# Performance work log

Hardware: AMD Instinct MI355X
Metric: run time of the kernel (lower is better)

## Reference

```python
import jax, jax.numpy as jnp
import numpy as np


def _dequantize_and_unpack(packed, scales):
    """packed: [d_out, d_in//2] int8, each byte holds two 4-bit nibbles.
    Returns [d_out, d_in] in scales.dtype, scaled per output row."""
    low = (packed & 15).astype(jnp.int8)
    high = (packed >> 4).astype(jnp.int8)  # arithmetic shift, like torch int8 >> 4
    low = jnp.where(low > 7, low - 16, low)
    high = jnp.where(high > 7, high - 16, high)
    # interleave: even cols = high nibble, odd cols = low nibble
    w = jnp.stack([high, low], axis=-1).reshape(packed.shape[0], -1)
    return w.astype(scales.dtype) * scales


def setup_inputs() -> dict:
    key = jax.random.key(0)
    ks = jax.random.split(key, 7)
    d = 4096
    N = 4096
    x = jax.random.normal(ks[0], (N, d), dtype=jnp.float32)
    fc1_weights_packed = jax.random.randint(ks[1], (2 * d, d // 2), -8, 7, dtype=jnp.int32).astype(jnp.int8)
    fc1_scales = (jax.random.normal(ks[2], (2 * d, 1), dtype=jnp.float32) * 0.02).astype(jnp.float16)
    fc1_bias = jax.random.normal(ks[3], (2 * d,), dtype=jnp.float32)
    fc2_weights_packed = jax.random.randint(ks[4], (d, d), -8, 7, dtype=jnp.int32).astype(jnp.int8)
    fc2_scales = (jax.random.normal(ks[5], (d, 1), dtype=jnp.float32) * 0.02).astype(jnp.float16)
    fc2_bias = jax.random.normal(ks[6], (d,), dtype=jnp.float32)
    return {
        "x": x,
        "fc1_weights_packed": fc1_weights_packed,
        "fc1_scales": fc1_scales,
        "fc1_bias": fc1_bias,
        "fc2_weights_packed": fc2_weights_packed,
        "fc2_scales": fc2_scales,
        "fc2_bias": fc2_bias,
    }


def reference(x, fc1_weights_packed, fc1_scales, fc1_bias,
              fc2_weights_packed, fc2_scales, fc2_bias):
    # fc1: dequantize to [2d, d], linear, relu
    w1 = _dequantize_and_unpack(fc1_weights_packed, fc1_scales).astype(x.dtype)
    h = jax.nn.relu(jnp.dot(x, w1.T) + fc1_bias)
    # fc2: dequantize to [d, 2d], linear
    w2 = _dequantize_and_unpack(fc2_weights_packed, fc2_scales).astype(x.dtype)
    return jnp.dot(h, w2.T) + fc2_bias
```

## Files before the change

### kernel.cpp

```cpp
#include <hip/hip_runtime.h>
#include <hip/hip_fp16.h>
#include <stdint.h>


typedef __attribute__((ext_vector_type(4)))  int i32x4;
typedef __attribute__((ext_vector_type(16))) int i32x16;
typedef __attribute__((ext_vector_type(8))) _Float16 f16x8;

__device__ __forceinline__ void load_lds16(const void* g, void* l) {
    __builtin_amdgcn_global_load_lds(
        (__attribute__((address_space(1))) void*)(void*)g,
        (__attribute__((address_space(3))) void*)(void*)l,
        16, 0, 0);
}

__device__ __forceinline__ float block_max(float m, int tid) {
    __shared__ float red[4];
#pragma unroll
    for (int off = 32; off; off >>= 1)
        m = fmaxf(m, __shfl_down(m, off, 64));
    if ((tid & 63) == 0) red[tid >> 6] = m;
    __syncthreads();
    m = fmaxf(fmaxf(red[0], red[1]), fmaxf(red[2], red[3]));
    __syncthreads();
    return m;
}

__global__ __launch_bounds__(256) void quant_x(
    const float* __restrict__ in, int* __restrict__ out,
    float* __restrict__ rscale, int ncols)
{
    const int tid = threadIdx.x;
    const int row = blockIdx.x;
    const float4* rp = (const float4*)(in + (size_t)row * ncols);
    const int nf4 = ncols / 4;
    float4 v[4];
    float m = 0.f;
#pragma unroll
    for (int k = 0; k < 4; ++k) {
        v[k] = rp[k * 256 + tid];
        m = fmaxf(m, fmaxf(fmaxf(fabsf(v[k].x), fabsf(v[k].y)),
                           fmaxf(fabsf(v[k].z), fabsf(v[k].w))));
    }
    m = block_max(m, tid);
    m = fmaxf(m, 1e-20f);
    const float inv = 127.f / m;
    if (tid == 0) rscale[row] = m / 127.f;
    int* orow = out + (size_t)row * nf4;
#pragma unroll
    for (int k = 0; k < 4; ++k) {
        int q0 = __float2int_rn(v[k].x * inv);
        int q1 = __float2int_rn(v[k].y * inv);
        int q2 = __float2int_rn(v[k].z * inv);
        int q3 = __float2int_rn(v[k].w * inv);
        orow[k * 256 + tid] = (q0 & 0xFF) | ((q1 & 0xFF) << 8) |
                              ((q2 & 0xFF) << 16) | ((q3 & 0xFF) << 24);
    }
}

__global__ __launch_bounds__(256) void quant_h(
    const _Float16* __restrict__ in, int2* __restrict__ out,
    float* __restrict__ rscale, int ncols)
{
    const int tid = threadIdx.x;
    const int row = blockIdx.x;
    const f16x8* rp = (const f16x8*)(in + (size_t)row * ncols);
    const int nv = ncols / 8;
    f16x8 v[4];
    float m = 0.f;
#pragma unroll
    for (int k = 0; k < 4; ++k) {
        v[k] = rp[k * 256 + tid];
#pragma unroll
        for (int e = 0; e < 8; ++e) m = fmaxf(m, (float)v[k][e]);
    }
    m = block_max(m, tid);
    m = fmaxf(m, 1e-20f);
    const float inv = 255.f / m;
    if (tid == 0) rscale[row] = m / 255.f;
    int2* orow = out + (size_t)row * nv;
#pragma unroll
    for (int k = 0; k < 4; ++k) {
        union { int8_t b[8]; int2 w; } u;
#pragma unroll
        for (int e = 0; e < 8; ++e) {
            int q = __float2int_rn((float)v[k][e] * inv);
            q = q < 0 ? 0 : (q > 255 ? 255 : q);
            u.b[e] = (int8_t)(q - 128);
        }
        orow[k * 256 + tid] = u.w;
    }
}

__global__ __launch_bounds__(256) void expand_int4_i8(
    const int4* __restrict__ packed, int2* __restrict__ out,
    int* __restrict__ wsum, int n_i4)
{
    const int tid = threadIdx.x;
    const int row = blockIdx.x;
    const int4* prow = packed + (size_t)row * n_i4;
    int2* orow = out + (size_t)row * n_i4;
    int sum = 0;
    for (int j = tid; j < n_i4; j += 256) {
        int4 p = prow[j];
        int vals[4] = {p.x, p.y, p.z, p.w};
        union { int8_t b[8]; int2 w; } u;
#pragma unroll
        for (int b = 0; b < 4; ++b) {
            int by = (int)(int8_t)(vals[b] & 0xFF);
            int hi = by >> 4;
            int lo = ((by & 15) ^ 8) - 8;
            u.b[2 * b] = (int8_t)hi;
            u.b[2 * b + 1] = (int8_t)lo;
            sum += hi + lo;
        }
        orow[j] = u.w;
    }
    __shared__ int sred[4];
#pragma unroll
    for (int off = 32; off; off >>= 1) sum += __shfl_down(sum, off, 64);
    if ((tid & 63) == 0) sred[tid >> 6] = sum;
    __syncthreads();
    if (tid == 0) wsum[row] = sred[0] + sred[1] + sred[2] + sred[3];
}

template <bool RELU, bool SHIFT, typename OutT>
__global__ __launch_bounds__(256) void gemm_i8(
    const int8_t* __restrict__ A, const int8_t* __restrict__ B,
    OutT* __restrict__ C,
    const float* __restrict__ sa,
    const float* __restrict__ s,
    const float* __restrict__ bias,
    const int* __restrict__ wsum,
    int M, int N, int K)
{
    __shared__ alignas(16) char sA[128 * 128];
    __shared__ alignas(16) char sB[128 * 128];

    const int tid  = threadIdx.x;
    const int lane = tid & 63;
    const int wave = tid >> 6;
    const int wm = wave & 1;
    const int wn = wave >> 1;

    const int bm = blockIdx.y * 128;
    const int bn = blockIdx.x * 128;

    const int srow = lane >> 3;
    const int scol = ((lane & 7) ^ srow) << 4;

    size_t goff[4];
    int    loff[4];
#pragma unroll
    for (int j = 0; j < 4; ++j) {
        const int c = j * 4 + wave;
        goff[j] = (size_t)(c * 8 + srow) * K + scol;
        loff[j] = c * 1024;
    }

    const int8_t* Ab = A + (size_t)bm * K;
    const int8_t* Bb = B + (size_t)bn * K;

    i32x16 acc[2][2] = {};

    const int l31 = lane & 31;
    const int kh  = lane >> 5;
    const int rsw = lane & 7;
    const char* sAc = (const char*)sA;
    const char* sBc = (const char*)sB;
    const int abase = (wm * 64 + l31) * 128;
    const int bbase = (wn * 64 + l31) * 128;

    for (int kt = 0; kt < K; kt += 128) {
#pragma unroll
        for (int j = 0; j < 4; ++j) {
            load_lds16(Ab + kt + goff[j], (char*)sA + loff[j]);
            load_lds16(Bb + kt + goff[j], (char*)sB + loff[j]);
        }
        __syncthreads();
#pragma unroll
        for (int ks = 0; ks < 4; ++ks) {
            const int coff = ((ks * 2 + kh) ^ rsw) * 16;
            i32x4 af[2], bf[2];
#pragma unroll
            for (int i = 0; i < 2; ++i) {
                af[i] = *(const i32x4*)(sAc + abase + i * 4096 + coff);
                bf[i] = *(const i32x4*)(sBc + bbase + i * 4096 + coff);
            }
#pragma unroll
            for (int i = 0; i < 2; ++i)
#pragma unroll
                for (int j = 0; j < 2; ++j)
                    acc[i][j] = __builtin_amdgcn_mfma_i32_32x32x32_i8(
                        af[i], bf[j], acc[i][j], 0, 0, 0);
        }
        __syncthreads();
    }

#pragma unroll
    for (int j = 0; j < 2; ++j) {
        const int n  = bn + wn * 64 + j * 32 + l31;
        const float sc = s[n];
        const float bs = bias[n];
        const int shf = SHIFT ? 128 * wsum[n] : 0;
#pragma unroll
        for (int i = 0; i < 2; ++i) {
            const int mb = bm + wm * 64 + i * 32 + 4 * kh;
#pragma unroll
            for (int reg = 0; reg < 16; ++reg) {
                const int m = mb + (reg & 3) + 8 * (reg >> 2);
                float v = (float)(acc[i][j][reg] + shf) * sc * sa[m] + bs;
                if (RELU) v = v > 0.f ? v : 0.f;
                C[(size_t)m * N + n] = (OutT)v;
            }
        }
    }
}

extern "C" void kernel_launch(void* const* d_in, const int* in_sizes, int n_in,
                              void* d_out, int out_size, void* d_ws, size_t ws_size,
                              hipStream_t stream)
{
    const float* x   = (const float*)d_in[0];
    const int4*  w1p = (const int4*)d_in[1];
    const float* s1  = (const float*)d_in[2];
    const float* b1  = (const float*)d_in[3];
    const int4*  w2p = (const int4*)d_in[4];
    const float* s2  = (const float*)d_in[5];
    const float* b2  = (const float*)d_in[6];
    float* out = (float*)d_out;

    const int d    = in_sizes[6];
    const int d2   = in_sizes[3];
    const int Ntok = in_sizes[0] / d;

    char* ws = (char*)d_ws;
    int8_t*   xq = (int8_t*)ws;
    int8_t*   wq = (int8_t*)(ws + (size_t)Ntok * d);
    _Float16* hb = (_Float16*)(ws + (size_t)Ntok * d + (size_t)d2 * d);
    int8_t*   hq = (int8_t*)((char*)hb + (size_t)Ntok * d2 * 2);
    float*    sx = (float*)((char*)hq + (size_t)Ntok * d2);
    float*    sh = sx + Ntok;
    int*      wsum = (int*)(sh + Ntok);

    quant_x<<<Ntok, 256, 0, stream>>>(x, (int*)xq, sx, d);
    expand_int4_i8<<<d2, 256, 0, stream>>>(w1p, (int2*)wq, wsum, d / 8);
    {
        dim3 grid(d2 / 128, Ntok / 128);
        gemm_i8<true, false, _Float16><<<grid, 256, 0, stream>>>(
            xq, wq, hb, sx, s1, b1, nullptr, Ntok, d2, d);
    }
    quant_h<<<Ntok, 256, 0, stream>>>(hb, (int2*)hq, sh, d2);
    expand_int4_i8<<<d, 256, 0, stream>>>(w2p, (int2*)wq, wsum, d2 / 8);
    {
        dim3 grid(d / 128, Ntok / 128);
        gemm_i8<false, true, float><<<grid, 256, 0, stream>>>(
            hq, wq, out, sh, s2, b2, wsum, Ntok, d, d2);
    }
}
```

Baseline: 513.5 us.

## Use 256x256 int8 GEMM tiles with double-buffered LDS and pipelined loads

Replaces the 128x128, 4-wave int8 GEMM with a 256x256, 8-wave kernel. It double-buffers A and B in LDS and issues the next tiles' async global-to-LDS loads between MFMA groups, using explicit waitcnt and barriers. It also adds setprio around MFMA bursts and an XCD-aware block remap. The aim is to hide global memory latency and raise arithmetic intensity per LDS byte, at the cost of 128KB of LDS per block and more complex synchronisation.

```diff
diff --git a/kernel.cpp b/kernel.cpp
--- a/kernel.cpp
+++ b/kernel.cpp
@@ -125,7 +125,7 @@
 }
 
 template <bool RELU, bool SHIFT, typename OutT>
-__global__ __launch_bounds__(256) void gemm_i8(
+__global__ __launch_bounds__(512, 2) void gemm_i8_256(
     const int8_t* __restrict__ A, const int8_t* __restrict__ B,
     OutT* __restrict__ C,
     const float* __restrict__ sa,
@@ -134,67 +134,118 @@
     const int* __restrict__ wsum,
     int M, int N, int K)
 {
-    __shared__ alignas(16) char sA[128 * 128];
-    __shared__ alignas(16) char sB[128 * 128];
+    __shared__ alignas(16) char sA[2][256 * 128];
+    __shared__ alignas(16) char sB[2][256 * 128];
 
     const int tid  = threadIdx.x;
     const int lane = tid & 63;
     const int wave = tid >> 6;
-    const int wm = wave & 1;
-    const int wn = wave >> 1;
-
-    const int bm = blockIdx.y * 128;
-    const int bn = blockIdx.x * 128;
-
-    const int srow = lane >> 3;
-    const int scol = ((lane & 7) ^ srow) << 4;
-
-    size_t goff[4];
-    int    loff[4];
-#pragma unroll
-    for (int j = 0; j < 4; ++j) {
-        const int c = j * 4 + wave;
-        goff[j] = (size_t)(c * 8 + srow) * K + scol;
-        loff[j] = c * 1024;
-    }
-
-    const int8_t* Ab = A + (size_t)bm * K;
-    const int8_t* Bb = B + (size_t)bn * K;
-
-    i32x16 acc[2][2] = {};
+    const int wm = wave >> 2;
+    const int wn = wave & 3;
+
+    const int nwg = gridDim.x * gridDim.y;
+    int bid = blockIdx.y * gridDim.x + blockIdx.x;
+    const int cpx = nwg >> 3;
+    bid = (bid & 7) * cpx + (bid >> 3);
+    const int bm = (bid / gridDim.x) * 256;
+    const int bn = (bid % gridDim.x) * 256;
+
+    const int srow = tid >> 3;
+    const int scol = ((tid & 7) ^ (srow & 7)) << 4;
+    const int8_t* Ag = A + (size_t)(bm + srow) * K + scol;
+    const int8_t* Bg = B + (size_t)(bn + srow) * K + scol;
+    const size_t rK64 = (size_t)64 * K;
+    const int ldst = tid * 16;
+
+    auto stage_a = [&](int buf, int h, int kt) {
+        const int8_t* g = Ag + (size_t)h * 128 * K + (size_t)kt * 128;
+        char* l = &sA[buf][h * 16384 + ldst];
+        load_lds16(g, l);
+        load_lds16(g + rK64, l + 8192);
+    };
+    auto stage_b = [&](int buf, int h, int kt) {
+        const int8_t* g = Bg + (size_t)h * 128 * K + (size_t)kt * 128;
+        char* l = &sB[buf][h * 16384 + ldst];
+        load_lds16(g, l);
+        load_lds16(g + rK64, l + 8192);
+    };
 
     const int l31 = lane & 31;
     const int kh  = lane >> 5;
-    const int rsw = lane & 7;
-    const char* sAc = (const char*)sA;
-    const char* sBc = (const char*)sB;
-    const int abase = (wm * 64 + l31) * 128;
-    const int bbase = (wn * 64 + l31) * 128;
-
-    for (int kt = 0; kt < K; kt += 128) {
-#pragma unroll
-        for (int j = 0; j < 4; ++j) {
-            load_lds16(Ab + kt + goff[j], (char*)sA + loff[j]);
-            load_lds16(Bb + kt + goff[j], (char*)sB + loff[j]);
-        }
-        __syncthreads();
-#pragma unroll
-        for (int ks = 0; ks < 4; ++ks) {
-            const int coff = ((ks * 2 + kh) ^ rsw) * 16;
-            i32x4 af[2], bf[2];
-#pragma unroll
-            for (int i = 0; i < 2; ++i) {
-                af[i] = *(const i32x4*)(sAc + abase + i * 4096 + coff);
-                bf[i] = *(const i32x4*)(sBc + bbase + i * 4096 + coff);
+    int coff[4];
+#pragma unroll
+    for (int ks = 0; ks < 4; ++ks)
+        coff[ks] = (((ks * 2 + kh) ^ (l31 & 7)) << 4);
+    int abase[4], bbase[2];
+#pragma unroll
+    for (int i = 0; i < 4; ++i) abase[i] = (wm * 128 + i * 32 + l31) * 128;
+#pragma unroll
+    for (int j = 0; j < 2; ++j) bbase[j] = (wn * 64 + j * 32 + l31) * 128;
+
+    i32x16 acc[4][2] = {};
+    const int NT = K >> 7;
+
+    stage_a(0, 0, 0); stage_a(0, 1, 0);
+    stage_b(0, 0, 0); stage_b(0, 1, 0);
+    if (NT > 1) { stage_b(1, 0, 1); stage_b(1, 1, 1); }
+
+    for (int t = 0; t < NT; ++t) {
+        const char* pA = sA[t & 1];
+        const char* pB = sB[t & 1];
+        if (t + 1 < NT) asm volatile("s_waitcnt vmcnt(4)" ::: "memory");
+        else            asm volatile("s_waitcnt vmcnt(0)" ::: "memory");
+        __builtin_amdgcn_s_barrier();
+        __builtin_amdgcn_sched_barrier(0);
+
+        i32x4 bf[2][4];
+        {
+            i32x4 af[4];
+#pragma unroll
+            for (int j = 0; j < 2; ++j)
+#pragma unroll
+                for (int ks = 0; ks < 4; ++ks)
+                    bf[j][ks] = *(const i32x4*)(pB + bbase[j] + coff[ks]);
+#pragma unroll
+            for (int ks = 0; ks < 4; ++ks)
+                af[ks] = *(const i32x4*)(pA + abase[0] + coff[ks]);
+            if (t + 1 < NT) stage_a((t + 1) & 1, 0, t + 1);
+            __builtin_amdgcn_s_barrier();
+            asm volatile("s_waitcnt lgkmcnt(0)" ::: "memory");
+            __builtin_amdgcn_sched_barrier(0);
+            __builtin_amdgcn_s_setprio(1);
+#pragma unroll
+            for (int ks = 0; ks < 4; ++ks) {
+                acc[0][0] = __builtin_amdgcn_mfma_i32_32x32x32_i8(
+                    af[ks], bf[0][ks], acc[0][0], 0, 0, 0);
+                acc[0][1] = __builtin_amdgcn_mfma_i32_32x32x32_i8(
+                    af[ks], bf[1][ks], acc[0][1], 0, 0, 0);
             }
-#pragma unroll
-            for (int i = 0; i < 2; ++i)
-#pragma unroll
-                for (int j = 0; j < 2; ++j)
-                    acc[i][j] = __builtin_amdgcn_mfma_i32_32x32x32_i8(
-                        af[i], bf[j], acc[i][j], 0, 0, 0);
-        }
-        __syncthreads();
+            __builtin_amdgcn_s_setprio(0);
+            __builtin_amdgcn_s_barrier();
+        }
+#pragma unroll
+        for (int i = 1; i < 4; ++i) {
+            i32x4 af[4];
+#pragma unroll
+            for (int ks = 0; ks < 4; ++ks)
+                af[ks] = *(const i32x4*)(pA + abase[i] + coff[ks]);
+            if (i == 1)      { if (t + 1 < NT) stage_a((t + 1) & 1, 1, t + 1); }
+            else if (i == 2) { if (t + 2 < NT) stage_b(t & 1, 0, t + 2); }
+            else             { if (t + 2 < NT) stage_b(t & 1, 1, t + 2); }
+            __builtin_amdgcn_s_barrier();
+            asm volatile("s_waitcnt lgkmcnt(0)" ::: "memory");
+            __builtin_amdgcn_sched_barrier(0);
+            __builtin_amdgcn_s_setprio(1);
+#pragma unroll
+            for (int ks = 0; ks < 4; ++ks) {
+                acc[i][0] = __builtin_amdgcn_mfma_i32_32x32x32_i8(
+                    af[ks], bf[0][ks], acc[i][0], 0, 0, 0);
+                acc[i][1] = __builtin_amdgcn_mfma_i32_32x32x32_i8(
+                    af[ks], bf[1][ks], acc[i][1], 0, 0, 0);
+            }
+            __builtin_amdgcn_s_setprio(0);
+            __builtin_amdgcn_s_barrier();
+        }
     }
 
 #pragma unroll
@@ -204,8 +255,8 @@
         const float bs = bias[n];
         const int shf = SHIFT ? 128 * wsum[n] : 0;
 #pragma unroll
-        for (int i = 0; i < 2; ++i) {
-            const int mb = bm + wm * 64 + i * 32 + 4 * kh;
+        for (int i = 0; i < 4; ++i) {
+            const int mb = bm + wm * 128 + i * 32 + 4 * kh;
 #pragma unroll
             for (int reg = 0; reg < 16; ++reg) {
                 const int m = mb + (reg & 3) + 8 * (reg >> 2);
@@ -246,15 +297,15 @@
     quant_x<<<Ntok, 256, 0, stream>>>(x, (int*)xq, sx, d);
     expand_int4_i8<<<d2, 256, 0, stream>>>(w1p, (int2*)wq, wsum, d / 8);
     {
-        dim3 grid(d2 / 128, Ntok / 128);
-        gemm_i8<true, false, _Float16><<<grid, 256, 0, stream>>>(
+        dim3 grid(d2 / 256, Ntok / 256);
+        gemm_i8_256<true, false, _Float16><<<grid, 512, 0, stream>>>(
             xq, wq, hb, sx, s1, b1, nullptr, Ntok, d2, d);
     }
     quant_h<<<Ntok, 256, 0, stream>>>(hb, (int2*)hq, sh, d2);
     expand_int4_i8<<<d, 256, 0, stream>>>(w2p, (int2*)wq, wsum, d2 / 8);
     {
-        dim3 grid(d / 128, Ntok / 128);
-        gemm_i8<false, true, float><<<grid, 256, 0, stream>>>(
+        dim3 grid(d / 256, Ntok / 256);
+        gemm_i8_256<false, true, float><<<grid, 512, 0, stream>>>(
             hq, wq, out, sh, s2, b2, wsum, Ntok, d, d2);
     }
 }
```

Result: no change. 519.9 us (+1.2%).

## Rewrite int8 GEMM with triple-buffered LDS pipeline, 128x256 tiles and XCD-aware block mapping

Applied to the files above, without the earlier changes.

Replaces the int8 MFMA GEMM with a 512-thread, 128x256-tile version that uses three LDS buffers of K=64 slices. Global-to-LDS loads run two tiles ahead, paced by explicit vmcnt/lgkmcnt waits and scheduling barriers so loads overlap MFMA work. Block indices are remapped so neighbouring N-tiles land on the same XCD, which aims to improve L2 reuse. The risks are the hand-tuned wait counts, lower occupancy from the larger tiles, and a bx mapping that assumes gridDim.x is a multiple of 8.

```diff
diff --git a/kernel.cpp b/kernel.cpp
--- a/kernel.cpp
+++ b/kernel.cpp
@@ -125,7 +125,7 @@
 }
 
 template <bool RELU, bool SHIFT, typename OutT>
-__global__ __launch_bounds__(256) void gemm_i8(
+__global__ __launch_bounds__(512, 4) void gemm_i8_v7(
     const int8_t* __restrict__ A, const int8_t* __restrict__ B,
     OutT* __restrict__ C,
     const float* __restrict__ sa,
@@ -134,73 +134,106 @@
     const int* __restrict__ wsum,
     int M, int N, int K)
 {
-    __shared__ alignas(16) char sA[128 * 128];
-    __shared__ alignas(16) char sB[128 * 128];
+    __shared__ alignas(1024) char sAB[3][24576];
 
     const int tid  = threadIdx.x;
     const int lane = tid & 63;
     const int wave = tid >> 6;
-    const int wm = wave & 1;
-    const int wn = wave >> 1;
-
-    const int bm = blockIdx.y * 128;
-    const int bn = blockIdx.x * 128;
-
-    const int srow = lane >> 3;
-    const int scol = ((lane & 7) ^ srow) << 4;
-
-    size_t goff[4];
-    int    loff[4];
-#pragma unroll
-    for (int j = 0; j < 4; ++j) {
-        const int c = j * 4 + wave;
-        goff[j] = (size_t)(c * 8 + srow) * K + scol;
-        loff[j] = c * 1024;
-    }
-
-    const int8_t* Ab = A + (size_t)bm * K;
-    const int8_t* Bb = B + (size_t)bn * K;
-
-    i32x16 acc[2][2] = {};
+    const int wm = wave >> 2;
+    const int wn = wave & 3;
+
+    int bid = blockIdx.y * gridDim.x + blockIdx.x;
+    const int xcd = bid & 7;
+    const int idx = bid >> 3;
+    const int cpx = gridDim.x >> 3;
+    const int bx = xcd * cpx + idx / gridDim.y;
+    const int by = idx % gridDim.y;
+    const int bm = by * 128;
+    const int bn = bx * 256;
+
+    const int srow = tid >> 2;
+    const int sq   = tid & 3;
+    const int sc   = sq ^ ((srow >> 1) & 3);
+    const int8_t* gA = A + (size_t)(bm + srow) * K + sc * 16;
+    const int8_t* gB = B + (size_t)(bn + srow) * K + sc * 16;
+    const size_t rK128 = (size_t)128 * K;
+    const int ldst = tid * 16;
 
     const int l31 = lane & 31;
     const int kh  = lane >> 5;
-    const int rsw = lane & 7;
-    const char* sAc = (const char*)sA;
-    const char* sBc = (const char*)sB;
-    const int abase = (wm * 64 + l31) * 128;
-    const int bbase = (wn * 64 + l31) * 128;
-
-    for (int kt = 0; kt < K; kt += 128) {
-#pragma unroll
-        for (int j = 0; j < 4; ++j) {
-            load_lds16(Ab + kt + goff[j], (char*)sA + loff[j]);
-            load_lds16(Bb + kt + goff[j], (char*)sB + loff[j]);
-        }
-        __syncthreads();
-#pragma unroll
-        for (int ks = 0; ks < 4; ++ks) {
-            const int coff = ((ks * 2 + kh) ^ rsw) * 16;
-            i32x4 af[2], bf[2];
-#pragma unroll
-            for (int i = 0; i < 2; ++i) {
-                af[i] = *(const i32x4*)(sAc + abase + i * 4096 + coff);
-                bf[i] = *(const i32x4*)(sBc + bbase + i * 4096 + coff);
-            }
-#pragma unroll
-            for (int i = 0; i < 2; ++i)
-#pragma unroll
-                for (int j = 0; j < 2; ++j)
-                    acc[i][j] = __builtin_amdgcn_mfma_i32_32x32x32_i8(
-                        af[i], bf[j], acc[i][j], 0, 0, 0);
-        }
-        __syncthreads();
-    }
+    const int ra  = wm * 64 + l31;
+    const int rb  = wn * 64 + l31;
+    const int aks0 = ra * 64 + (((0 + kh) ^ ((ra >> 1) & 3)) << 4);
+    const int aks1 = ra * 64 + (((2 + kh) ^ ((ra >> 1) & 3)) << 4);
+    const int bks0 = 8192 + rb * 64 + (((0 + kh) ^ ((rb >> 1) & 3)) << 4);
+    const int bks1 = 8192 + rb * 64 + (((2 + kh) ^ ((rb >> 1) & 3)) << 4);
+
+    i32x4 afX[2], afY[2], bfX[2], bfY[2];
+    i32x16 acc[2][2] = {};
+    const int NT = K >> 6;
+
+#define SB0() __builtin_amdgcn_sched_barrier(0)
+#define STAGE(P, kt)                                                        \
+    do { const size_t ko = (size_t)(kt) * 64;                               \
+        load_lds16(gA + ko, &sAB[P][ldst]);                                 \
+        load_lds16(gB + ko, &sAB[P][8192 + ldst]);                          \
+        load_lds16(gB + ko + rK128, &sAB[P][16384 + ldst]); } while (0)
+#define READF(P)                                                            \
+    do { const char* p_ = sAB[P];                                           \
+        afX[0] = *(const i32x4*)(p_ + aks0);                                \
+        afX[1] = *(const i32x4*)(p_ + aks0 + 2048);                         \
+        bfX[0] = *(const i32x4*)(p_ + bks0);                                \
+        bfX[1] = *(const i32x4*)(p_ + bks0 + 2048);                         \
+        afY[0] = *(const i32x4*)(p_ + aks1);                                \
+        afY[1] = *(const i32x4*)(p_ + aks1 + 2048);                         \
+        bfY[0] = *(const i32x4*)(p_ + bks1);                                \
+        bfY[1] = *(const i32x4*)(p_ + bks1 + 2048); } while (0)
+#define MFMA4(AF, BF)                                                       \
+    do { _Pragma("unroll")                                                  \
+        for (int i_ = 0; i_ < 2; ++i_) {                                    \
+            acc[i_][0] = __builtin_amdgcn_mfma_i32_32x32x32_i8(             \
+                AF[i_], BF[0], acc[i_][0], 0, 0, 0);                        \
+            acc[i_][1] = __builtin_amdgcn_mfma_i32_32x32x32_i8(             \
+                AF[i_], BF[1], acc[i_][1], 0, 0, 0);                        \
+        } } while (0)
+#define TILE(u, P)                                                          \
+    if ((u) < NT) {                                                         \
+        if ((u) + 1 < NT) asm volatile("s_waitcnt vmcnt(3)" ::: "memory");  \
+        else              asm volatile("s_waitcnt vmcnt(0)" ::: "memory");  \
+        SB0();                                                              \
+        __builtin_amdgcn_s_barrier();                                       \
+        SB0();                                                              \
+        if ((u) + 2 < NT) STAGE((P + 2) % 3, (u) + 2);                      \
+        SB0();                                                              \
+        READF(P);                                                           \
+        SB0();                                                              \
+        asm volatile("s_waitcnt lgkmcnt(4)" ::: "memory");                  \
+        SB0();                                                              \
+        MFMA4(afX, bfX);                                                    \
+        SB0();                                                              \
+        asm volatile("s_waitcnt lgkmcnt(0)" ::: "memory");                  \
+        SB0();                                                              \
+        MFMA4(afY, bfY);                                                    \
+    }
+
+    STAGE(0, 0);
+    if (NT > 1) STAGE(1, 1);
+
+    for (int t = 0; t < NT; t += 3) {
+        TILE(t,     0);
+        TILE(t + 1, 1);
+        TILE(t + 2, 2);
+    }
+#undef SB0
+#undef STAGE
+#undef READF
+#undef MFMA4
+#undef TILE
 
 #pragma unroll
     for (int j = 0; j < 2; ++j) {
         const int n  = bn + wn * 64 + j * 32 + l31;
-        const float sc = s[n];
+        const float sc2 = s[n];
         const float bs = bias[n];
         const int shf = SHIFT ? 128 * wsum[n] : 0;
 #pragma unroll
@@ -209,7 +242,7 @@
 #pragma unroll
             for (int reg = 0; reg < 16; ++reg) {
                 const int m = mb + (reg & 3) + 8 * (reg >> 2);
-                float v = (float)(acc[i][j][reg] + shf) * sc * sa[m] + bs;
+                float v = (float)(acc[i][j][reg] + shf) * sc2 * sa[m] + bs;
                 if (RELU) v = v > 0.f ? v : 0.f;
                 C[(size_t)m * N + n] = (OutT)v;
             }
@@ -246,15 +279,15 @@
     quant_x<<<Ntok, 256, 0, stream>>>(x, (int*)xq, sx, d);
     expand_int4_i8<<<d2, 256, 0, stream>>>(w1p, (int2*)wq, wsum, d / 8);
     {
-        dim3 grid(d2 / 128, Ntok / 128);
-        gemm_i8<true, false, _Float16><<<grid, 256, 0, stream>>>(
+        dim3 grid(d2 / 256, Ntok / 128);
+        gemm_i8_v7<true, false, _Float16><<<grid, 512, 0, stream>>>(
             xq, wq, hb, sx, s1, b1, nullptr, Ntok, d2, d);
     }
     quant_h<<<Ntok, 256, 0, stream>>>(hb, (int2*)hq, sh, d2);
     expand_int4_i8<<<d, 256, 0, stream>>>(w2p, (int2*)wq, wsum, d2 / 8);
     {
-        dim3 grid(d / 128, Ntok / 128);
-        gemm_i8<false, true, float><<<grid, 256, 0, stream>>>(
+        dim3 grid(d / 256, Ntok / 128);
+        gemm_i8_v7<false, true, float><<<grid, 512, 0, stream>>>(
             hq, wq, out, sh, s2, b2, wsum, Ntok, d, d2);
     }
 }
```

Measured after the change: 527.8 us. 2.8% more time.
